# Kernel tuning notes

Measured on AMD Instinct MI355X. Metric: run time of the kernel, lower is better.

The kernel has to match this reference:

```python
import jax, jax.numpy as jnp
import numpy as np

EPS_BN = 1e-5
NEG_SLOPE = 0.1
NUM_HEADS = 4


def _normalize(x):
    n = jnp.linalg.norm(x, axis=-1, keepdims=True)
    return x / jnp.maximum(n, 1e-12)


def _bn(x):
    # training-mode BatchNorm over all dims except channel (gamma=1, beta=0 at init)
    axes = tuple(range(x.ndim - 1))
    m = jnp.mean(x, axis=axes, keepdims=True)
    v = jnp.var(x, axis=axes, keepdims=True)
    return (x - m) * jax.lax.rsqrt(v + EPS_BN)


def _linear_bn(x, w, b):
    return _bn(x @ w.T + b)


def _gather(points, idx):
    # points [B,N,C], idx [B,M,K] -> [B,M,K,C]
    B = points.shape[0]
    return points[jnp.arange(B)[:, None, None], idx]


def _vi_transform(localized, g_norm, s_norm):
    # localized, g_norm: [B,M,K,3]; s_norm: [B,M,3]
    sn = s_norm[:, :, None, :]                                   # [B,M,1,3]
    r_hat = _normalize(localized)
    dot = lambda a, b: jnp.sum(a * b, axis=-1, keepdims=True)
    proj = dot(sn, r_hat)                                        # [B,M,K,1]
    v_miu = _normalize(sn - proj * r_hat)
    w_miu = _normalize(jnp.cross(r_hat, v_miu))
    t1 = dot(g_norm, sn)
    t2 = proj
    t3 = dot(r_hat, g_norm)
    t4 = dot(localized, sn)
    t5 = dot(g_norm, r_hat)
    t6 = dot(g_norm, v_miu)
    t7 = dot(g_norm, w_miu)
    t8 = dot(localized, jnp.cross(g_norm, jnp.broadcast_to(sn, g_norm.shape)))
    t9 = jnp.linalg.norm(localized, axis=-1, keepdims=True)
    return jnp.concatenate([t1, t2, t3, t4, t5, t6, t7, t8, t9, localized], axis=-1)  # [B,M,K,12]


def setup_inputs() -> dict:
    key = jax.random.key(0)
    B, N, M, K = 2, 100000, 25000, 16
    C_IN, C_OUT, GF, WN = 64, 128, 32, 16
    C4 = C_OUT // 4
    ks = jax.random.split(key, 32)
    s = 0.05
    d = {
        'dense_xyz': jax.random.normal(ks[0], (B, N, 3), jnp.float32),
        'sparse_xyz': jax.random.normal(ks[1], (B, M, 3), jnp.float32),
        'dense_feats': jax.random.normal(ks[2], (B, N, C_IN), jnp.float32),
        'dense_xyz_norm': _normalize(jax.random.normal(ks[3], (B, N, 3), jnp.float32)),
        'sparse_xyz_norm': _normalize(jax.random.normal(ks[4], (B, M, 3), jnp.float32)),
        'mlp_conv_w': jax.random.normal(ks[5], (GF, 12), jnp.float32) * s,
        'mlp_conv_b': jnp.zeros((GF,), jnp.float32),
        'gu_w': jax.random.normal(ks[6], (GF, GF), jnp.float32) * s,
        'gu_b': jnp.zeros((GF,), jnp.float32),
        'gm0_w': jax.random.normal(ks[7], (8, GF), jnp.float32) * s,
        'gm0_b': jnp.zeros((8,), jnp.float32),
        'gm1_w': jax.random.normal(ks[8], (NUM_HEADS, 8), jnp.float32) * s,
        'gm1_b': jnp.zeros((NUM_HEADS,), jnp.float32),
        'u1_w': jax.random.normal(ks[9], (C4, C_IN), jnp.float32) * s,
        'u1_b': jnp.zeros((C4,), jnp.float32),
        'wn0_w': jax.random.normal(ks[10], (8, 12), jnp.float32) * s,
        'wn0_b': jnp.zeros((8,), jnp.float32),
        'wn1_w': jax.random.normal(ks[11], (8, 8), jnp.float32) * s,
        'wn1_b': jnp.zeros((8,), jnp.float32),
        'wn2_w': jax.random.normal(ks[12], (WN, 8), jnp.float32) * s,
        'wn2_b': jnp.zeros((WN,), jnp.float32),
        'u2_w': jax.random.normal(ks[13], (C_OUT, C4 * WN), jnp.float32) * s,
        'u2_b': jnp.zeros((C_OUT,), jnp.float32),
        'us_w': jax.random.normal(ks[14], (C_OUT, C_IN), jnp.float32) * s,
        'us_b': jnp.zeros((C_OUT,), jnp.float32),
        'nei_inds': jax.random.randint(ks[15], (B, M, K), 0, N, jnp.int32),
    }
    return d


def reference(dense_xyz, sparse_xyz, dense_feats, dense_xyz_norm, sparse_xyz_norm,
              mlp_conv_w, mlp_conv_b, gu_w, gu_b, gm0_w, gm0_b, gm1_w, gm1_b,
              u1_w, u1_b, wn0_w, wn0_b, wn1_w, wn1_b, wn2_w, wn2_b,
              u2_w, u2_b, us_w, us_b, nei_inds):
    # neighbor gather + localize
    g_xyz = _gather(dense_xyz, nei_inds)                       # [B,M,K,3]
    localized = g_xyz - sparse_xyz[:, :, None, :]
    g_norm = _gather(dense_xyz_norm, nei_inds)
    vi = _vi_transform(localized, g_norm, sparse_xyz_norm)     # [B,M,K,12]

    # guidance branch
    feat_pe = jax.nn.relu(_linear_bn(vi, mlp_conv_w, mlp_conv_b))      # [B,M,K,GF]
    guidance = _linear_bn(feat_pe, gu_w, gu_b)                          # no relu
    g_key = jnp.max(guidance, axis=2, keepdims=True)                    # [B,M,1,GF]
    sc = jax.nn.relu(_linear_bn(guidance - g_key, gm0_w, gm0_b))
    scores = jax.nn.sigmoid(sc @ gm1_w.T + gm1_b)                       # [B,M,K,H]

    # feature branch
    feats_x = jax.nn.leaky_relu(_linear_bn(dense_feats, u1_w, u1_b), NEG_SLOPE)  # [B,N,C/4]
    gf = _gather(feats_x, nei_inds)                                     # [B,M,K,C4]
    B, M, K, C = gf.shape
    gf = (gf.reshape(B, M, K, NUM_HEADS, C // NUM_HEADS) * scores[..., None]).reshape(B, M, K, C)

    # WeightNet on VI features
    w = vi
    for ww, wb in ((wn0_w, wn0_b), (wn1_w, wn1_b), (wn2_w, wn2_b)):
        w = jax.nn.relu(_linear_bn(w, ww, wb))                          # [B,M,K,WN]

    new_feat = jnp.einsum('bmkc,bmkw->bmcw', gf, w).reshape(B, M, -1)   # [B,M,C4*WN]
    new_feat = _linear_bn(new_feat, u2_w, u2_b)                         # [B,M,C_OUT], no relu

    # shortcut: max-pool gathered input feats
    shortcut = _linear_bn(jnp.max(_gather(dense_feats, nei_inds), axis=2), us_w, us_b)
    return jax.nn.leaky_relu(new_feat + shortcut, NEG_SLOPE)
```

## Files before the change

### kernel.cpp

```cpp
#include <hip/hip_runtime.h>
#include <math.h>

constexpr int Bq = 2;
constexpr int Nq = 100000;
constexpr int Mq = 25000;
constexpr int Kq = 16;

constexpr size_t OFF_Y8  = 0;
constexpr size_t OFF_VI  = 25600000;
constexpr size_t OFF_DS  = 64000000;
constexpr size_t OFF_FS  = OFF_DS + 8192;
constexpr size_t OFF_WC  = OFF_DS + 16384;

constexpr int G_BN1 = 0;
constexpr int G_BN5 = 64;
constexpr int G_BN4 = 80;
constexpr int G_BN2 = 144;
constexpr int G_BN6 = 208;
constexpr int G_BN3 = 224;
constexpr int G_BN7 = 240;
constexpr int G_BN8 = 272;
constexpr int G_BN9 = 528;

struct P {
  const float *dxyz,*sxyz,*dfeat,*dnorm,*snorm;
  const float *w_mlp,*b_mlp,*w_gu,*b_gu,*w_gm0,*b_gm0,*w_gm1,*b_gm1;
  const float *w_u1,*b_u1,*w_wn0,*b_wn0,*w_wn1,*b_wn1,*w_wn2,*b_wn2;
  const float *w_u2,*b_u2,*w_us,*b_us;
  const int* nei;
  float* vi; float* y8; float* y9; double* ds; float* fs;
  float* wc; float* out;
};

__device__ __forceinline__ float lrelu(float x){ return x > 0.f ? x : 0.1f*x; }

__device__ __forceinline__ void load_vi(const P& p, int row, float v[12]){
  const float4* vp = (const float4*)(p.vi + (size_t)row*12);
  float4 a = vp[0], b = vp[1], c = vp[2];
  v[0]=a.x; v[1]=a.y; v[2]=a.z; v[3]=a.w;
  v[4]=b.x; v[5]=b.y; v[6]=b.z; v[7]=b.w;
  v[8]=c.x; v[9]=c.y; v[10]=c.z; v[11]=c.w;
}
__device__ __forceinline__ void featpe(const P& p, const float v[12], float fp[32]){
  #pragma unroll
  for (int c = 0; c < 32; c++){
    float y = p.b_mlp[c];
    #pragma unroll
    for (int j = 0; j < 12; j++) y += p.w_mlp[c*12+j]*v[j];
    fp[c] = fmaxf((y - p.fs[G_BN1+c])*p.fs[G_BN1+32+c], 0.f);
  }
}
__device__ __forceinline__ void wchain0(const P& p, const float v[12], float w0[8]){
  #pragma unroll
  for (int c = 0; c < 8; c++){
    float y = p.b_wn0[c];
    #pragma unroll
    for (int j = 0; j < 12; j++) y += p.w_wn0[c*12+j]*v[j];
    w0[c] = fmaxf((y - p.fs[G_BN5+c])*p.fs[G_BN5+8+c], 0.f);
  }
}

__global__ __launch_bounds__(256) void k_tr(P p){
  int i = blockIdx.x*256 + threadIdx.x;
  if (i < 576*128){
    int d = i >> 7, o = i & 127;
    p.wc[i] = (d < 512) ? p.w_u2[(size_t)o*512 + d] : p.w_us[(size_t)o*64 + (d-512)];
  }
}

__global__ __launch_bounds__(256) void k_vi(P p){
  __shared__ float ls[80];
  int t = threadIdx.x;
  if (t < 80) ls[t] = 0.f;
  __syncthreads();

  float a1[32], q1[32], a5[8], q5[8];
  #pragma unroll
  for (int c = 0; c < 32; c++){ a1[c]=0.f; q1[c]=0.f; }
  #pragma unroll
  for (int c = 0; c < 8; c++){ a5[c]=0.f; q5[c]=0.f; }

  int base = blockIdx.x*1280 + t;
  for (int r = 0; r < 5; r++){
    int row = base + r*256;
    int b   = row / (Mq*Kq);
    int rem = row - b*(Mq*Kq);
    int m   = rem >> 4;
    int bm  = b*Mq + m;
    int idx = p.nei[row];

    const float* gx = p.dxyz  + ((size_t)b*Nq + idx)*3;
    const float* gn = p.dnorm + ((size_t)b*Nq + idx)*3;
    const float* sx = p.sxyz  + (size_t)bm*3;
    const float* sn = p.snorm + (size_t)bm*3;

    float lx = gx[0]-sx[0], ly = gx[1]-sx[1], lz = gx[2]-sx[2];
    float gnx = gn[0], gny = gn[1], gnz = gn[2];
    float snx = sn[0], sny = sn[1], snz = sn[2];

    float rn = sqrtf(lx*lx + ly*ly + lz*lz);
    float rd = fmaxf(rn, 1e-12f);
    float rx = lx/rd, ry = ly/rd, rz = lz/rd;
    float proj = snx*rx + sny*ry + snz*rz;
    float vx = snx - proj*rx, vy = sny - proj*ry, vz = snz - proj*rz;
    float vn = sqrtf(vx*vx + vy*vy + vz*vz);
    float vd = fmaxf(vn, 1e-12f);
    vx /= vd; vy /= vd; vz /= vd;
    float wx = ry*vz - rz*vy, wy = rz*vx - rx*vz, wz = rx*vy - ry*vx;
    float wnn = sqrtf(wx*wx + wy*wy + wz*wz);
    float wd = fmaxf(wnn, 1e-12f);
    wx /= wd; wy /= wd; wz /= wd;
    float cx = gny*snz - gnz*sny, cy = gnz*snx - gnx*snz, cz = gnx*sny - gny*snx;

    float v[12];
    v[0] = gnx*snx + gny*sny + gnz*snz;
    v[1] = proj;
    v[2] = rx*gnx + ry*gny + rz*gnz;
    v[3] = lx*snx + ly*sny + lz*snz;
    v[4] = v[2];
    v[5] = gnx*vx + gny*vy + gnz*vz;
    v[6] = gnx*wx + gny*wy + gnz*wz;
    v[7] = lx*cx + ly*cy + lz*cz;
    v[8] = rn;
    v[9] = lx; v[10] = ly; v[11] = lz;

    float4* vo = (float4*)(p.vi + (size_t)row*12);
    vo[0] = make_float4(v[0],v[1],v[2],v[3]);
    vo[1] = make_float4(v[4],v[5],v[6],v[7]);
    vo[2] = make_float4(v[8],v[9],v[10],v[11]);

    #pragma unroll
    for (int c = 0; c < 32; c++){
      float y = p.b_mlp[c];
      #pragma unroll
      for (int j = 0; j < 12; j++) y += p.w_mlp[c*12 + j]*v[j];
      a1[c] += y; q1[c] += y*y;
    }
    #pragma unroll
    for (int c = 0; c < 8; c++){
      float y = p.b_wn0[c];
      #pragma unroll
      for (int j = 0; j < 12; j++) y += p.w_wn0[c*12 + j]*v[j];
      a5[c] += y; q5[c] += y*y;
    }
  }
  int lane = t & 63;
  #pragma unroll
  for (int i = 0; i < 32; i++){
    int c = (lane + i) & 31;
    atomicAdd(&ls[c], a1[c]); atomicAdd(&ls[32+c], q1[c]);
  }
  #pragma unroll
  for (int i = 0; i < 8; i++){
    int c = (lane + i) & 7;
    atomicAdd(&ls[64+c], a5[c]); atomicAdd(&ls[72+c], q5[c]);
  }
  __syncthreads();
  if (t < 32){
    atomicAdd(&p.ds[G_BN1+t], (double)ls[t]);
    atomicAdd(&p.ds[G_BN1+32+t], (double)ls[32+t]);
  } else if (t < 40){
    int c = t - 32;
    atomicAdd(&p.ds[G_BN5+c], (double)ls[64+c]);
    atomicAdd(&p.ds[G_BN5+8+c], (double)ls[72+c]);
  }
}

__global__ __launch_bounds__(256) void k_u1s(P p){
  __shared__ float ls[64];
  int t = threadIdx.x;
  if (t < 64) ls[t] = 0.f;
  __syncthreads();
  float a4[32], q4[32];
  #pragma unroll
  for (int c = 0; c < 32; c++){ a4[c]=0.f; q4[c]=0.f; }
  int base = blockIdx.x*1280 + t;
  for (int r = 0; r < 5; r++){
    int row = base + r*256;
    if (row < Bq*Nq){
      const float4* f4 = (const float4*)(p.dfeat + (size_t)row*64);
      float fr[64];
      #pragma unroll
      for (int q = 0; q < 16; q++){
        float4 x = f4[q];
        fr[q*4+0]=x.x; fr[q*4+1]=x.y; fr[q*4+2]=x.z; fr[q*4+3]=x.w;
      }
      #pragma unroll
      for (int c = 0; c < 32; c++){
        float y = p.b_u1[c];
        #pragma unroll
        for (int j = 0; j < 64; j++) y += p.w_u1[c*64 + j]*fr[j];
        a4[c] += y; q4[c] += y*y;
      }
    }
  }
  int lane = t & 63;
  #pragma unroll
  for (int i = 0; i < 32; i++){
    int c = (lane + i) & 31;
    atomicAdd(&ls[c], a4[c]); atomicAdd(&ls[32+c], q4[c]);
  }
  __syncthreads();
  if (t < 32){
    atomicAdd(&p.ds[G_BN4+t], (double)ls[t]);
    atomicAdd(&p.ds[G_BN4+32+t], (double)ls[32+t]);
  }
}

__device__ __forceinline__ void fin_group(const double* ds, float* fs, int off, int C, double n){
  for (int c = threadIdx.x; c < C; c += blockDim.x){
    double s = ds[off+c], q = ds[off+C+c];
    double mu = s/n;
    double va = q/n - mu*mu;
    if (va < 0.0) va = 0.0;
    fs[off+c]   = (float)mu;
    fs[off+C+c] = 1.f/sqrtf((float)va + 1e-5f);
  }
}
__global__ void k_fin1(P p){ fin_group(p.ds,p.fs,G_BN1,32,800000.0); fin_group(p.ds,p.fs,G_BN5,8,800000.0); fin_group(p.ds,p.fs,G_BN4,32,200000.0); }
__global__ void k_fin2(P p){ fin_group(p.ds,p.fs,G_BN2,32,800000.0); fin_group(p.ds,p.fs,G_BN6,8,800000.0); }
__global__ void k_fin3(P p){ fin_group(p.ds,p.fs,G_BN3,8,800000.0);  fin_group(p.ds,p.fs,G_BN7,16,800000.0); }
__global__ void k_fin4(P p){ fin_group(p.ds,p.fs,G_BN8,128,50000.0); fin_group(p.ds,p.fs,G_BN9,128,50000.0); }

__global__ __launch_bounds__(256) void k_s2(P p){
  __shared__ float ls[80];
  int t = threadIdx.x;
  if (t < 80) ls[t] = 0.f;
  __syncthreads();
  float a2[32], q2[32], a6[8], q6[8];
  #pragma unroll
  for (int c = 0; c < 32; c++){ a2[c]=0.f; q2[c]=0.f; }
  #pragma unroll
  for (int c = 0; c < 8; c++){ a6[c]=0.f; q6[c]=0.f; }
  int base = blockIdx.x*1280 + t;
  for (int r = 0; r < 5; r++){
    int row = base + r*256;
    float v[12]; load_vi(p, row, v);
    float fp[32]; featpe(p, v, fp);
    #pragma unroll
    for (int c = 0; c < 32; c++){
      float y = p.b_gu[c];
      #pragma unroll
      for (int j = 0; j < 32; j++) y += p.w_gu[c*32+j]*fp[j];
      a2[c] += y; q2[c] += y*y;
    }
    float w0[8]; wchain0(p, v, w0);
    #pragma unroll
    for (int c = 0; c < 8; c++){
      float y = p.b_wn1[c];
      #pragma unroll
      for (int j = 0; j < 8; j++) y += p.w_wn1[c*8+j]*w0[j];
      a6[c] += y; q6[c] += y*y;
    }
  }
  int lane = t & 63;
  #pragma unroll
  for (int i = 0; i < 32; i++){
    int c = (lane + i) & 31;
    atomicAdd(&ls[c], a2[c]); atomicAdd(&ls[32+c], q2[c]);
  }
  #pragma unroll
  for (int i = 0; i < 8; i++){
    int c = (lane + i) & 7;
    atomicAdd(&ls[64+c], a6[c]); atomicAdd(&ls[72+c], q6[c]);
  }
  __syncthreads();
  if (t < 32){
    atomicAdd(&p.ds[G_BN2+t], (double)ls[t]);
    atomicAdd(&p.ds[G_BN2+32+t], (double)ls[32+t]);
  } else if (t < 40){
    int c = t - 32;
    atomicAdd(&p.ds[G_BN6+c], (double)ls[64+c]);
    atomicAdd(&p.ds[G_BN6+8+c], (double)ls[72+c]);
  }
}

__global__ __launch_bounds__(256) void k_s3(P p){
  __shared__ float ls[48];
  int t = threadIdx.x;
  if (t < 48) ls[t] = 0.f;
  __syncthreads();
  int lane = t & 63;
  int k  = lane & 15;
  int pl = (t >> 6)*4 + (lane >> 4);
  float a3[8], q3[8], a7[16], q7[16];
  #pragma unroll
  for (int c = 0; c < 8; c++){ a3[c]=0.f; q3[c]=0.f; }
  #pragma unroll
  for (int c = 0; c < 16; c++){ a7[c]=0.f; q7[c]=0.f; }

  for (int it = 0; it < 5; it++){
    int pg = blockIdx.x*80 + it*16 + pl;
    int row = pg*16 + k;
    float v[12]; load_vi(p, row, v);
    float fp[32]; featpe(p, v, fp);
    float g[32];
    #pragma unroll
    for (int c = 0; c < 32; c++){
      float y = p.b_gu[c];
      #pragma unroll
      for (int j = 0; j < 32; j++) y += p.w_gu[c*32+j]*fp[j];
      g[c] = (y - p.fs[G_BN2+c])*p.fs[G_BN2+32+c];
    }
    #pragma unroll
    for (int c = 0; c < 32; c++){
      float mx = g[c];
      mx = fmaxf(mx, __shfl_xor(mx, 1, 16));
      mx = fmaxf(mx, __shfl_xor(mx, 2, 16));
      mx = fmaxf(mx, __shfl_xor(mx, 4, 16));
      mx = fmaxf(mx, __shfl_xor(mx, 8, 16));
      g[c] -= mx;
    }
    #pragma unroll
    for (int c = 0; c < 8; c++){
      float y = p.b_gm0[c];
      #pragma unroll
      for (int j = 0; j < 32; j++) y += p.w_gm0[c*32+j]*g[j];
      a3[c] += y; q3[c] += y*y;
    }
    float w0[8]; wchain0(p, v, w0);
    float w1[8];
    #pragma unroll
    for (int c = 0; c < 8; c++){
      float y = p.b_wn1[c];
      #pragma unroll
      for (int j = 0; j < 8; j++) y += p.w_wn1[c*8+j]*w0[j];
      w1[c] = fmaxf((y - p.fs[G_BN6+c])*p.fs[G_BN6+8+c], 0.f);
    }
    #pragma unroll
    for (int c = 0; c < 16; c++){
      float y = p.b_wn2[c];
      #pragma unroll
      for (int j = 0; j < 8; j++) y += p.w_wn2[c*8+j]*w1[j];
      a7[c] += y; q7[c] += y*y;
    }
  }
  #pragma unroll
  for (int i = 0; i < 8; i++){
    int c = (lane + i) & 7;
    atomicAdd(&ls[c], a3[c]); atomicAdd(&ls[8+c], q3[c]);
  }
  #pragma unroll
  for (int i = 0; i < 16; i++){
    int c = (lane + i) & 15;
    atomicAdd(&ls[16+c], a7[c]); atomicAdd(&ls[32+c], q7[c]);
  }
  __syncthreads();
  if (t < 8){
    atomicAdd(&p.ds[G_BN3+t], (double)ls[t]);
    atomicAdd(&p.ds[G_BN3+8+t], (double)ls[8+t]);
  } else if (t < 24){
    int c = t - 8;
    atomicAdd(&p.ds[G_BN7+c], (double)ls[16+c]);
    atomicAdd(&p.ds[G_BN7+16+c], (double)ls[32+c]);
  }
}

__global__ __launch_bounds__(256) void k_chain2(P p){
  __shared__ __align__(16) float sb[16*592];
  __shared__ float ls[512];
  int t = threadIdx.x;
  ls[t] = 0.f; ls[t+256] = 0.f;

  int lane = t & 63;
  int k  = lane & 15;
  int pl = (t >> 6)*4 + (lane >> 4);
  int pg = blockIdx.x*16 + pl;
  int b  = pg / Mq;
  int row = pg*16 + k;
  float* sp = &sb[pl*592];

  float v[12]; load_vi(p, row, v);
  float fp[32]; featpe(p, v, fp);
  float g[32];
  #pragma unroll
  for (int c = 0; c < 32; c++){
    float y = p.b_gu[c];
    #pragma unroll
    for (int j = 0; j < 32; j++) y += p.w_gu[c*32+j]*fp[j];
    g[c] = (y - p.fs[G_BN2+c])*p.fs[G_BN2+32+c];
  }
  #pragma unroll
  for (int c = 0; c < 32; c++){
    float mx = g[c];
    mx = fmaxf(mx, __shfl_xor(mx, 1, 16));
    mx = fmaxf(mx, __shfl_xor(mx, 2, 16));
    mx = fmaxf(mx, __shfl_xor(mx, 4, 16));
    mx = fmaxf(mx, __shfl_xor(mx, 8, 16));
    g[c] -= mx;
  }
  float sc[8];
  #pragma unroll
  for (int c = 0; c < 8; c++){
    float y = p.b_gm0[c];
    #pragma unroll
    for (int j = 0; j < 32; j++) y += p.w_gm0[c*32+j]*g[j];
    sc[c] = fmaxf((y - p.fs[G_BN3+c])*p.fs[G_BN3+8+c], 0.f);
  }
  float scr[4];
  #pragma unroll
  for (int h = 0; h < 4; h++){
    float y = p.b_gm1[h];
    #pragma unroll
    for (int j = 0; j < 8; j++) y += p.w_gm1[h*8+j]*sc[j];
    scr[h] = 1.f/(1.f + expf(-y));
  }
  float w0[8]; wchain0(p, v, w0);
  float w1[8];
  #pragma unroll
  for (int c = 0; c < 8; c++){
    float y = p.b_wn1[c];
    #pragma unroll
    for (int j = 0; j < 8; j++) y += p.w_wn1[c*8+j]*w0[j];
    w1[c] = fmaxf((y - p.fs[G_BN6+c])*p.fs[G_BN6+8+c], 0.f);
  }
  float wv[16];
  #pragma unroll
  for (int c = 0; c < 16; c++){
    float y = p.b_wn2[c];
    #pragma unroll
    for (int j = 0; j < 8; j++) y += p.w_wn2[c*8+j]*w1[j];
    wv[c] = fmaxf((y - p.fs[G_BN7+c])*p.fs[G_BN7+16+c], 0.f);
  }

  int idx = p.nei[row];
  const float4* f4 = (const float4*)(p.dfeat + ((size_t)b*Nq + idx)*64);
  float fr[64];
  #pragma unroll
  for (int q = 0; q < 16; q++){
    float4 x = f4[q];
    fr[q*4+0]=x.x; fr[q*4+1]=x.y; fr[q*4+2]=x.z; fr[q*4+3]=x.w;
  }
  #pragma unroll
  for (int c = 0; c < 32; c++){
    float y = p.b_u1[c];
    #pragma unroll
    for (int j = 0; j < 64; j++) y += p.w_u1[c*64+j]*fr[j];
    float fx = lrelu((y - p.fs[G_BN4+c])*p.fs[G_BN4+32+c]);
    sp[k*33 + c] = fx*scr[c >> 3];
  }
  float sx0=0.f, sx1=0.f, sx2=0.f, sx3=0.f;
  #pragma unroll
  for (int q = 0; q < 16; q++){
    float m0=fr[q*4+0], m1=fr[q*4+1], m2=fr[q*4+2], m3=fr[q*4+3];
    m0=fmaxf(m0,__shfl_xor(m0,1,16)); m0=fmaxf(m0,__shfl_xor(m0,2,16)); m0=fmaxf(m0,__shfl_xor(m0,4,16)); m0=fmaxf(m0,__shfl_xor(m0,8,16));
    m1=fmaxf(m1,__shfl_xor(m1,1,16)); m1=fmaxf(m1,__shfl_xor(m1,2,16)); m1=fmaxf(m1,__shfl_xor(m1,4,16)); m1=fmaxf(m1,__shfl_xor(m1,8,16));
    m2=fmaxf(m2,__shfl_xor(m2,1,16)); m2=fmaxf(m2,__shfl_xor(m2,2,16)); m2=fmaxf(m2,__shfl_xor(m2,4,16)); m2=fmaxf(m2,__shfl_xor(m2,8,16));
    m3=fmaxf(m3,__shfl_xor(m3,1,16)); m3=fmaxf(m3,__shfl_xor(m3,2,16)); m3=fmaxf(m3,__shfl_xor(m3,4,16)); m3=fmaxf(m3,__shfl_xor(m3,8,16));
    if (q == k){ sx0=m0; sx1=m1; sx2=m2; sx3=m3; }
  }
  __syncthreads();

  float ga[16], gb[16];
  #pragma unroll
  for (int kp = 0; kp < 16; kp++){
    ga[kp] = sp[kp*33 + k];
    gb[kp] = sp[kp*33 + k + 16];
  }
  __syncthreads();

  {
    float4* d4p = (float4*)&sp[k*20];
    d4p[0] = make_float4(wv[0],wv[1],wv[2],wv[3]);
    d4p[1] = make_float4(wv[4],wv[5],wv[6],wv[7]);
    d4p[2] = make_float4(wv[8],wv[9],wv[10],wv[11]);
    d4p[3] = make_float4(wv[12],wv[13],wv[14],wv[15]);
  }
  __syncthreads();

  float nf0[16], nf1[16];
  #pragma unroll
  for (int wi = 0; wi < 16; wi++){ nf0[wi]=0.f; nf1[wi]=0.f; }
  #pragma unroll 4
  for (int kp = 0; kp < 16; kp++){
    const float4* wp = (const float4*)&sp[kp*20];
    float4 wa = wp[0], wb = wp[1], wc = wp[2], wd = wp[3];
    float wvv[16] = {wa.x,wa.y,wa.z,wa.w, wb.x,wb.y,wb.z,wb.w,
                     wc.x,wc.y,wc.z,wc.w, wd.x,wd.y,wd.z,wd.w};
    #pragma unroll
    for (int wi = 0; wi < 16; wi++){
      nf0[wi] += ga[kp]*wvv[wi];
      nf1[wi] += gb[kp]*wvv[wi];
    }
  }
  __syncthreads();

  {
    float4* na = (float4*)&sp[k*16];
    na[0] = make_float4(nf0[0],nf0[1],nf0[2],nf0[3]);
    na[1] = make_float4(nf0[4],nf0[5],nf0[6],nf0[7]);
    na[2] = make_float4(nf0[8],nf0[9],nf0[10],nf0[11]);
    na[3] = make_float4(nf0[12],nf0[13],nf0[14],nf0[15]);
    float4* nb = (float4*)&sp[(k+16)*16];
    nb[0] = make_float4(nf1[0],nf1[1],nf1[2],nf1[3]);
    nb[1] = make_float4(nf1[4],nf1[5],nf1[6],nf1[7]);
    nb[2] = make_float4(nf1[8],nf1[9],nf1[10],nf1[11]);
    nb[3] = make_float4(nf1[12],nf1[13],nf1[14],nf1[15]);
    *(float4*)&sp[512 + k*4] = make_float4(sx0,sx1,sx2,sx3);
  }
  __syncthreads();

  int o   = t & 127;
  int ptg = t >> 7;
  float acc[8];
  #pragma unroll
  for (int i = 0; i < 8; i++) acc[i] = 0.f;
  #pragma unroll 2
  for (int d4 = 0; d4 < 128; d4++){
    const float* wr = p.wc + (size_t)(d4*4)*128 + o;
    float wa = wr[0], wb = wr[128], wcv = wr[256], wd = wr[384];
    #pragma unroll
    for (int i = 0; i < 8; i++){
      float4 av = *(const float4*)&sb[(ptg*8+i)*592 + d4*4];
      acc[i] += av.x*wa + av.y*wb + av.z*wcv + av.w*wd;
    }
  }
  float ac9[8];
  #pragma unroll
  for (int i = 0; i < 8; i++) ac9[i] = 0.f;
  #pragma unroll
  for (int d4 = 128; d4 < 144; d4++){
    const float* wr = p.wc + (size_t)(d4*4)*128 + o;
    float wa = wr[0], wb = wr[128], wcv = wr[256], wd = wr[384];
    #pragma unroll
    for (int i = 0; i < 8; i++){
      float4 av = *(const float4*)&sb[(ptg*8+i)*592 + d4*4];
      ac9[i] += av.x*wa + av.y*wb + av.z*wcv + av.w*wd;
    }
  }

  float bu2 = p.b_u2[o], bus = p.b_us[o];
  size_t obase = (size_t)(blockIdx.x*16)*128 + o;
  float s8=0.f, q8=0.f, s9=0.f, q9=0.f;
  #pragma unroll
  for (int i = 0; i < 8; i++){
    int pt = ptg*8 + i;
    float y8v = acc[i] + bu2;
    float y9v = ac9[i] + bus;
    p.y8[obase + (size_t)pt*128] = y8v;
    p.y9[obase + (size_t)pt*128] = y9v;
    s8 += y8v; q8 += y8v*y8v;
    s9 += y9v; q9 += y9v*y9v;
  }
  atomicAdd(&ls[o], s8);      atomicAdd(&ls[128+o], q8);
  atomicAdd(&ls[256+o], s9);  atomicAdd(&ls[384+o], q9);
  __syncthreads();
  atomicAdd(&p.ds[G_BN8+t], (double)ls[t]);
  atomicAdd(&p.ds[G_BN9+t], (double)ls[256+t]);
}

__global__ __launch_bounds__(256) void k_out(P p){
  size_t i = ((size_t)blockIdx.x*256 + threadIdx.x)*4;
  int c = (int)(i & 127);
  float4 a  = *(const float4*)(p.y8 + i);
  float4 b4 = *(const float4*)(p.y9 + i);
  const float* m8 = p.fs + G_BN8;  const float* i8 = p.fs + G_BN8 + 128;
  const float* m9 = p.fs + G_BN9;  const float* i9 = p.fs + G_BN9 + 128;
  float r0 = lrelu((a.x - m8[c  ])*i8[c  ] + (b4.x - m9[c  ])*i9[c  ]);
  float r1 = lrelu((a.y - m8[c+1])*i8[c+1] + (b4.y - m9[c+1])*i9[c+1]);
  float r2 = lrelu((a.z - m8[c+2])*i8[c+2] + (b4.z - m9[c+2])*i9[c+2]);
  float r3 = lrelu((a.w - m8[c+3])*i8[c+3] + (b4.w - m9[c+3])*i9[c+3]);
  *(float4*)(p.out + i) = make_float4(r0,r1,r2,r3);
}

extern "C" void kernel_launch(void* const* d_in, const int* in_sizes, int n_in,
                              void* d_out, int out_size, void* d_ws, size_t ws_size,
                              hipStream_t stream){
  (void)in_sizes; (void)n_in; (void)out_size; (void)ws_size;
  P p;
  p.dxyz  = (const float*)d_in[0];
  p.sxyz  = (const float*)d_in[1];
  p.dfeat = (const float*)d_in[2];
  p.dnorm = (const float*)d_in[3];
  p.snorm = (const float*)d_in[4];
  p.w_mlp = (const float*)d_in[5];  p.b_mlp = (const float*)d_in[6];
  p.w_gu  = (const float*)d_in[7];  p.b_gu  = (const float*)d_in[8];
  p.w_gm0 = (const float*)d_in[9];  p.b_gm0 = (const float*)d_in[10];
  p.w_gm1 = (const float*)d_in[11]; p.b_gm1 = (const float*)d_in[12];
  p.w_u1  = (const float*)d_in[13]; p.b_u1  = (const float*)d_in[14];
  p.w_wn0 = (const float*)d_in[15]; p.b_wn0 = (const float*)d_in[16];
  p.w_wn1 = (const float*)d_in[17]; p.b_wn1 = (const float*)d_in[18];
  p.w_wn2 = (const float*)d_in[19]; p.b_wn2 = (const float*)d_in[20];
  p.w_u2  = (const float*)d_in[21]; p.b_u2  = (const float*)d_in[22];
  p.w_us  = (const float*)d_in[23]; p.b_us  = (const float*)d_in[24];
  p.nei   = (const int*)d_in[25];
  char* ws = (char*)d_ws;
  p.y8  = (float*)(ws + OFF_Y8);
  p.vi  = (float*)(ws + OFF_VI);
  p.y9  = (float*)d_out;
  p.ds  = (double*)(ws + OFF_DS);
  p.fs  = (float*)(ws + OFF_FS);
  p.wc  = (float*)(ws + OFF_WC);
  p.out = (float*)d_out;

  hipMemsetAsync(ws + OFF_DS, 0, 784*sizeof(double), stream);

  k_tr    <<< 288, 256, 0, stream>>>(p);
  k_vi    <<< 625, 256, 0, stream>>>(p);
  k_u1s   <<< 157, 256, 0, stream>>>(p);
  k_fin1  <<<   1, 128, 0, stream>>>(p);
  k_s2    <<< 625, 256, 0, stream>>>(p);
  k_fin2  <<<   1, 128, 0, stream>>>(p);
  k_s3    <<< 625, 256, 0, stream>>>(p);
  k_fin3  <<<   1, 128, 0, stream>>>(p);
  k_chain2<<<3125, 256, 0, stream>>>(p);
  k_fin4  <<<   1, 128, 0, stream>>>(p);
  k_out   <<<6250, 256, 0, stream>>>(p);
}
```

Before: 1.394 ms.

## Materialize intermediate activations to avoid recomputing MLP chains in later passes

The first statistics pass (k_s2) now stores the guidance rows with their per-neighborhood max already subtracted, plus the WeightNet layer-1 pre-activations. k_u1s stores the u1 projection of every dense point, and a new k_fx kernel applies BN and leaky-ReLU to it. Later passes (k_s3, chain2) load these buffers instead of recomputing the VI-feature MLP, the guidance MLP and the 64x32 u1 projection per gathered neighbor. Because the BN mean cancels after subtracting the max, only the rstd scale is applied, which is exact. The cost is roughly 130 MB of extra workspace writes and reads, with new buffers placed in reused workspace regions (fx overlays vi, y4 overlays y8).

```diff
diff --git a/kernel.cpp b/kernel.cpp
--- a/kernel.cpp
+++ b/kernel.cpp
@@ -8,7 +8,9 @@
 
 constexpr size_t OFF_Y8  = 0;
 constexpr size_t OFF_VI  = 25600000;
-constexpr size_t OFF_DS  = 64000000;
+constexpr size_t OFF_ZC  = 64000000;
+constexpr size_t OFF_W1P = 166400000;
+constexpr size_t OFF_DS  = 192000000;
 constexpr size_t OFF_FS  = OFF_DS + 8192;
 constexpr size_t OFF_WC  = OFF_DS + 16384;
 
@@ -29,7 +31,7 @@
   const float *w_u2,*b_u2,*w_us,*b_us;
   const int* nei;
   float* vi; float* y8; float* y9; double* ds; float* fs;
-  float* wc; float* out;
+  float* wc; float* zc; float* w1p; float* y4; float* fx; float* out;
 };
 
 __device__ __forceinline__ float lrelu(float x){ return x > 0.f ? x : 0.1f*x; }
@@ -185,12 +187,16 @@
         float4 x = f4[q];
         fr[q*4+0]=x.x; fr[q*4+1]=x.y; fr[q*4+2]=x.z; fr[q*4+3]=x.w;
       }
+      float zb[4];
       #pragma unroll
       for (int c = 0; c < 32; c++){
         float y = p.b_u1[c];
         #pragma unroll
         for (int j = 0; j < 64; j++) y += p.w_u1[c*64 + j]*fr[j];
         a4[c] += y; q4[c] += y*y;
+        zb[c & 3] = y;
+        if ((c & 3) == 3)
+          *(float4*)(p.y4 + (size_t)row*32 + (c-3)) = make_float4(zb[0],zb[1],zb[2],zb[3]);
       }
     }
   }
@@ -227,33 +233,50 @@
   int t = threadIdx.x;
   if (t < 80) ls[t] = 0.f;
   __syncthreads();
+  int lane = t & 63;
+  int k  = lane & 15;
+  int pl = (t >> 6)*4 + (lane >> 4);
   float a2[32], q2[32], a6[8], q6[8];
   #pragma unroll
   for (int c = 0; c < 32; c++){ a2[c]=0.f; q2[c]=0.f; }
   #pragma unroll
   for (int c = 0; c < 8; c++){ a6[c]=0.f; q6[c]=0.f; }
-  int base = blockIdx.x*1280 + t;
-  for (int r = 0; r < 5; r++){
-    int row = base + r*256;
+
+  for (int it = 0; it < 5; it++){
+    int pg = blockIdx.x*80 + it*16 + pl;
+    int row = pg*16 + k;
     float v[12]; load_vi(p, row, v);
     float fp[32]; featpe(p, v, fp);
+    float zb[4];
     #pragma unroll
     for (int c = 0; c < 32; c++){
       float y = p.b_gu[c];
       #pragma unroll
       for (int j = 0; j < 32; j++) y += p.w_gu[c*32+j]*fp[j];
       a2[c] += y; q2[c] += y*y;
+      float mx = y;
+      mx = fmaxf(mx, __shfl_xor(mx, 1, 16));
+      mx = fmaxf(mx, __shfl_xor(mx, 2, 16));
+      mx = fmaxf(mx, __shfl_xor(mx, 4, 16));
+      mx = fmaxf(mx, __shfl_xor(mx, 8, 16));
+      zb[c & 3] = y - mx;
+      if ((c & 3) == 3)
+        *(float4*)(p.zc + (size_t)row*32 + (c-3)) = make_float4(zb[0],zb[1],zb[2],zb[3]);
     }
     float w0[8]; wchain0(p, v, w0);
+    float wb[8];
     #pragma unroll
     for (int c = 0; c < 8; c++){
       float y = p.b_wn1[c];
       #pragma unroll
       for (int j = 0; j < 8; j++) y += p.w_wn1[c*8+j]*w0[j];
       a6[c] += y; q6[c] += y*y;
-    }
-  }
-  int lane = t & 63;
+      wb[c] = y;
+    }
+    float4* wp = (float4*)(p.w1p + (size_t)row*8);
+    wp[0] = make_float4(wb[0],wb[1],wb[2],wb[3]);
+    wp[1] = make_float4(wb[4],wb[5],wb[6],wb[7]);
+  }
   #pragma unroll
   for (int i = 0; i < 32; i++){
     int c = (lane + i) & 31;
@@ -275,41 +298,42 @@
   }
 }
 
+__global__ __launch_bounds__(256) void k_fx(P p){
+  int gid = blockIdx.x*256 + threadIdx.x;
+  size_t i = (size_t)gid*4;
+  int c = (int)(i & 31);
+  float4 y = *(const float4*)(p.y4 + i);
+  float4 r;
+  r.x = lrelu((y.x - p.fs[G_BN4+c  ])*p.fs[G_BN4+32+c  ]);
+  r.y = lrelu((y.y - p.fs[G_BN4+c+1])*p.fs[G_BN4+32+c+1]);
+  r.z = lrelu((y.z - p.fs[G_BN4+c+2])*p.fs[G_BN4+32+c+2]);
+  r.w = lrelu((y.w - p.fs[G_BN4+c+3])*p.fs[G_BN4+32+c+3]);
+  *(float4*)(p.fx + i) = r;
+}
+
 __global__ __launch_bounds__(256) void k_s3(P p){
   __shared__ float ls[48];
   int t = threadIdx.x;
   if (t < 48) ls[t] = 0.f;
   __syncthreads();
-  int lane = t & 63;
-  int k  = lane & 15;
-  int pl = (t >> 6)*4 + (lane >> 4);
   float a3[8], q3[8], a7[16], q7[16];
   #pragma unroll
   for (int c = 0; c < 8; c++){ a3[c]=0.f; q3[c]=0.f; }
   #pragma unroll
   for (int c = 0; c < 16; c++){ a7[c]=0.f; q7[c]=0.f; }
 
-  for (int it = 0; it < 5; it++){
-    int pg = blockIdx.x*80 + it*16 + pl;
-    int row = pg*16 + k;
-    float v[12]; load_vi(p, row, v);
-    float fp[32]; featpe(p, v, fp);
+  int base = blockIdx.x*1280 + t;
+  for (int r = 0; r < 5; r++){
+    int row = base + r*256;
     float g[32];
-    #pragma unroll
-    for (int c = 0; c < 32; c++){
-      float y = p.b_gu[c];
-      #pragma unroll
-      for (int j = 0; j < 32; j++) y += p.w_gu[c*32+j]*fp[j];
-      g[c] = (y - p.fs[G_BN2+c])*p.fs[G_BN2+32+c];
-    }
-    #pragma unroll
-    for (int c = 0; c < 32; c++){
-      float mx = g[c];
-      mx = fmaxf(mx, __shfl_xor(mx, 1, 16));
-      mx = fmaxf(mx, __shfl_xor(mx, 2, 16));
-      mx = fmaxf(mx, __shfl_xor(mx, 4, 16));
-      mx = fmaxf(mx, __shfl_xor(mx, 8, 16));
-      g[c] -= mx;
+    const float4* zp = (const float4*)(p.zc + (size_t)row*32);
+    #pragma unroll
+    for (int q = 0; q < 8; q++){
+      float4 z = zp[q];
+      g[q*4+0] = z.x*p.fs[G_BN2+32+q*4+0];
+      g[q*4+1] = z.y*p.fs[G_BN2+32+q*4+1];
+      g[q*4+2] = z.z*p.fs[G_BN2+32+q*4+2];
+      g[q*4+3] = z.w*p.fs[G_BN2+32+q*4+3];
     }
     #pragma unroll
     for (int c = 0; c < 8; c++){
@@ -318,15 +342,12 @@
       for (int j = 0; j < 32; j++) y += p.w_gm0[c*32+j]*g[j];
       a3[c] += y; q3[c] += y*y;
     }
-    float w0[8]; wchain0(p, v, w0);
-    float w1[8];
-    #pragma unroll
-    for (int c = 0; c < 8; c++){
-      float y = p.b_wn1[c];
-      #pragma unroll
-      for (int j = 0; j < 8; j++) y += p.w_wn1[c*8+j]*w0[j];
-      w1[c] = fmaxf((y - p.fs[G_BN6+c])*p.fs[G_BN6+8+c], 0.f);
-    }
+    const float4* wp = (const float4*)(p.w1p + (size_t)row*8);
+    float4 wa = wp[0], wbv = wp[1];
+    float w1[8] = {wa.x,wa.y,wa.z,wa.w, wbv.x,wbv.y,wbv.z,wbv.w};
+    #pragma unroll
+    for (int c = 0; c < 8; c++)
+      w1[c] = fmaxf((w1[c] - p.fs[G_BN6+c])*p.fs[G_BN6+8+c], 0.f);
     #pragma unroll
     for (int c = 0; c < 16; c++){
       float y = p.b_wn2[c];
@@ -335,6 +356,7 @@
       a7[c] += y; q7[c] += y*y;
     }
   }
+  int lane = t & 63;
   #pragma unroll
   for (int i = 0; i < 8; i++){
     int c = (lane + i) & 7;
@@ -370,24 +392,17 @@
   int row = pg*16 + k;
   float* sp = &sb[pl*592];
 
-  float v[12]; load_vi(p, row, v);
-  float fp[32]; featpe(p, v, fp);
   float g[32];
-  #pragma unroll
-  for (int c = 0; c < 32; c++){
-    float y = p.b_gu[c];
-    #pragma unroll
-    for (int j = 0; j < 32; j++) y += p.w_gu[c*32+j]*fp[j];
-    g[c] = (y - p.fs[G_BN2+c])*p.fs[G_BN2+32+c];
-  }
-  #pragma unroll
-  for (int c = 0; c < 32; c++){
-    float mx = g[c];
-    mx = fmaxf(mx, __shfl_xor(mx, 1, 16));
-    mx = fmaxf(mx, __shfl_xor(mx, 2, 16));
-    mx = fmaxf(mx, __shfl_xor(mx, 4, 16));
-    mx = fmaxf(mx, __shfl_xor(mx, 8, 16));
-    g[c] -= mx;
+  {
+    const float4* zp = (const float4*)(p.zc + (size_t)row*32);
+    #pragma unroll
+    for (int q = 0; q < 8; q++){
+      float4 z = zp[q];
+      g[q*4+0] = z.x*p.fs[G_BN2+32+q*4+0];
+      g[q*4+1] = z.y*p.fs[G_BN2+32+q*4+1];
+      g[q*4+2] = z.z*p.fs[G_BN2+32+q*4+2];
+      g[q*4+3] = z.w*p.fs[G_BN2+32+q*4+3];
+    }
   }
   float sc[8];
   #pragma unroll
@@ -405,49 +420,54 @@
     for (int j = 0; j < 8; j++) y += p.w_gm1[h*8+j]*sc[j];
     scr[h] = 1.f/(1.f + expf(-y));
   }
-  float w0[8]; wchain0(p, v, w0);
-  float w1[8];
-  #pragma unroll
-  for (int c = 0; c < 8; c++){
-    float y = p.b_wn1[c];
-    #pragma unroll
-    for (int j = 0; j < 8; j++) y += p.w_wn1[c*8+j]*w0[j];
-    w1[c] = fmaxf((y - p.fs[G_BN6+c])*p.fs[G_BN6+8+c], 0.f);
-  }
   float wv[16];
-  #pragma unroll
-  for (int c = 0; c < 16; c++){
-    float y = p.b_wn2[c];
-    #pragma unroll
-    for (int j = 0; j < 8; j++) y += p.w_wn2[c*8+j]*w1[j];
-    wv[c] = fmaxf((y - p.fs[G_BN7+c])*p.fs[G_BN7+16+c], 0.f);
+  {
+    const float4* wp = (const float4*)(p.w1p + (size_t)row*8);
+    float4 wa = wp[0], wbv = wp[1];
+    float w1[8] = {wa.x,wa.y,wa.z,wa.w, wbv.x,wbv.y,wbv.z,wbv.w};
+    #pragma unroll
+    for (int c = 0; c < 8; c++)
+      w1[c] = fmaxf((w1[c] - p.fs[G_BN6+c])*p.fs[G_BN6+8+c], 0.f);
+    #pragma unroll
+    for (int c = 0; c < 16; c++){
+      float y = p.b_wn2[c];
+      #pragma unroll
+      for (int j = 0; j < 8; j++) y += p.w_wn2[c*8+j]*w1[j];
+      wv[c] = fmaxf((y - p.fs[G_BN7+c])*p.fs[G_BN7+16+c], 0.f);
+    }
   }
 
   int idx = p.nei[row];
-  const float4* f4 = (const float4*)(p.dfeat + ((size_t)b*Nq + idx)*64);
-  float fr[64];
-  #pragma unroll
-  for (int q = 0; q < 16; q++){
-    float4 x = f4[q];
-    fr[q*4+0]=x.x; fr[q*4+1]=x.y; fr[q*4+2]=x.z; fr[q*4+3]=x.w;
-  }
-  #pragma unroll
-  for (int c = 0; c < 32; c++){
-    float y = p.b_u1[c];
-    #pragma unroll
-    for (int j = 0; j < 64; j++) y += p.w_u1[c*64+j]*fr[j];
-    float fx = lrelu((y - p.fs[G_BN4+c])*p.fs[G_BN4+32+c]);
-    sp[k*33 + c] = fx*scr[c >> 3];
+  {
+    const float4* x4 = (const float4*)(p.fx + ((size_t)b*Nq + idx)*32);
+    #pragma unroll
+    for (int q = 0; q < 8; q++){
+      float4 x = x4[q];
+      int c = q*4;
+      sp[k*33 + c  ] = x.x*scr[c>>3];
+      sp[k*33 + c+1] = x.y*scr[c>>3];
+      sp[k*33 + c+2] = x.z*scr[c>>3];
+      sp[k*33 + c+3] = x.w*scr[c>>3];
+    }
   }
   float sx0=0.f, sx1=0.f, sx2=0.f, sx3=0.f;
-  #pragma unroll
-  for (int q = 0; q < 16; q++){
-    float m0=fr[q*4+0], m1=fr[q*4+1], m2=fr[q*4+2], m3=fr[q*4+3];
-    m0=fmaxf(m0,__shfl_xor(m0,1,16)); m0=fmaxf(m0,__shfl_xor(m0,2,16)); m0=fmaxf(m0,__shfl_xor(m0,4,16)); m0=fmaxf(m0,__shfl_xor(m0,8,16));
-    m1=fmaxf(m1,__shfl_xor(m1,1,16)); m1=fmaxf(m1,__shfl_xor(m1,2,16)); m1=fmaxf(m1,__shfl_xor(m1,4,16)); m1=fmaxf(m1,__shfl_xor(m1,8,16));
-    m2=fmaxf(m2,__shfl_xor(m2,1,16)); m2=fmaxf(m2,__shfl_xor(m2,2,16)); m2=fmaxf(m2,__shfl_xor(m2,4,16)); m2=fmaxf(m2,__shfl_xor(m2,8,16));
-    m3=fmaxf(m3,__shfl_xor(m3,1,16)); m3=fmaxf(m3,__shfl_xor(m3,2,16)); m3=fmaxf(m3,__shfl_xor(m3,4,16)); m3=fmaxf(m3,__shfl_xor(m3,8,16));
-    if (q == k){ sx0=m0; sx1=m1; sx2=m2; sx3=m3; }
+  {
+    const float4* f4 = (const float4*)(p.dfeat + ((size_t)b*Nq + idx)*64);
+    float fr[64];
+    #pragma unroll
+    for (int q = 0; q < 16; q++){
+      float4 x = f4[q];
+      fr[q*4+0]=x.x; fr[q*4+1]=x.y; fr[q*4+2]=x.z; fr[q*4+3]=x.w;
+    }
+    #pragma unroll
+    for (int q = 0; q < 16; q++){
+      float m0=fr[q*4+0], m1=fr[q*4+1], m2=fr[q*4+2], m3=fr[q*4+3];
+      m0=fmaxf(m0,__shfl_xor(m0,1,16)); m0=fmaxf(m0,__shfl_xor(m0,2,16)); m0=fmaxf(m0,__shfl_xor(m0,4,16)); m0=fmaxf(m0,__shfl_xor(m0,8,16));
+      m1=fmaxf(m1,__shfl_xor(m1,1,16)); m1=fmaxf(m1,__shfl_xor(m1,2,16)); m1=fmaxf(m1,__shfl_xor(m1,4,16)); m1=fmaxf(m1,__shfl_xor(m1,8,16));
+      m2=fmaxf(m2,__shfl_xor(m2,1,16)); m2=fmaxf(m2,__shfl_xor(m2,2,16)); m2=fmaxf(m2,__shfl_xor(m2,4,16)); m2=fmaxf(m2,__shfl_xor(m2,8,16));
+      m3=fmaxf(m3,__shfl_xor(m3,1,16)); m3=fmaxf(m3,__shfl_xor(m3,2,16)); m3=fmaxf(m3,__shfl_xor(m3,4,16)); m3=fmaxf(m3,__shfl_xor(m3,8,16));
+      if (q == k){ sx0=m0; sx1=m1; sx2=m2; sx3=m3; }
+    }
   }
   __syncthreads();
 
@@ -586,7 +606,11 @@
   p.nei   = (const int*)d_in[25];
   char* ws = (char*)d_ws;
   p.y8  = (float*)(ws + OFF_Y8);
+  p.y4  = (float*)(ws + OFF_Y8);
   p.vi  = (float*)(ws + OFF_VI);
+  p.fx  = (float*)(ws + OFF_VI);
+  p.zc  = (float*)(ws + OFF_ZC);
+  p.w1p = (float*)(ws + OFF_W1P);
   p.y9  = (float*)d_out;
   p.ds  = (double*)(ws + OFF_DS);
   p.fs  = (float*)(ws + OFF_FS);
@@ -600,6 +624,7 @@
   k_u1s   <<< 157, 256, 0, stream>>>(p);
   k_fin1  <<<   1, 128, 0, stream>>>(p);
   k_s2    <<< 625, 256, 0, stream>>>(p);
+  k_fx    <<<6250, 256, 0, stream>>>(p);
   k_fin2  <<<   1, 128, 0, stream>>>(p);
   k_s3    <<< 625, 256, 0, stream>>>(p);
   k_fin3  <<<   1, 128, 0, stream>>>(p);
```

Result: faster. 1.201 ms (-13.9%).
